# Kernel tuning notes

Measured on AMD Instinct MI355X. Metric: run time of the kernel, lower is better.

The kernel has to match this reference:

```python
import jax, jax.numpy as jnp
import numpy as np

D = 256   # dim = vis_dim = key_channels = value_channels = audio_dim
BT = 64   # batch*time
H = 64
W = 64
L = 32    # audio length

_CONV_NAMES = ["vis_project", "av", "vv", "vo", "ao", "vs_key", "vs_q1", "vs_q2",
               "as_key", "as_q1", "as_q2", "outconv", "aoc"]


def _conv1(x, w, b):
    # pointwise Conv1d: x [B,C,Lx], w [O,C], b [O]
    return jnp.einsum('oc,bcl->bol', w, x) + b[None, :, None]


def _inorm(x, eps=1e-5):
    # InstanceNorm1d (affine=False): normalize over last (spatial) axis
    m = jnp.mean(x, axis=-1, keepdims=True)
    v = jnp.var(x, axis=-1, keepdims=True)
    return (x - m) * jax.lax.rsqrt(v + eps)


def _gelu(x):
    return jax.nn.gelu(x, approximate=False)


def setup_inputs() -> dict:
    key = jax.random.key(0)
    ks = jax.random.split(key, 40)
    inp = {
        "x": jax.random.normal(ks[0], (BT, D, H, W), jnp.float32),
        "audio": jax.random.normal(ks[1], (BT, D, L), jnp.float32),
        "audio_mask": jnp.ones((BT, L, 1), jnp.float32),
    }
    for i, n in enumerate(_CONV_NAMES):
        inp[n + "_w"] = jax.random.normal(ks[3 + 2 * i], (D, D), jnp.float32) * 0.05
        inp[n + "_b"] = jax.random.normal(ks[4 + 2 * i], (D,), jnp.float32) * 0.01
    inp["gate_w1"] = jax.random.normal(ks[30], (D, D), jnp.float32) * 0.05
    inp["gate_w2"] = jax.random.normal(ks[31], (D, D), jnp.float32) * 0.05
    inp["vis_weight"] = jnp.ones((1,), jnp.float32)
    inp["audio_weight"] = jnp.ones((1,), jnp.float32)
    return inp


def reference(x, audio, audio_mask,
              vis_project_w, vis_project_b, av_w, av_b, vv_w, vv_b, vo_w, vo_b,
              ao_w, ao_b, vs_key_w, vs_key_b, vs_q1_w, vs_q1_b, vs_q2_w, vs_q2_b,
              as_key_w, as_key_b, as_q1_w, as_q1_b, as_q2_w, as_q2_b,
              outconv_w, outconv_b, aoc_w, aoc_b, gate_w1, gate_w2,
              vis_weight, audio_weight):
    bt, c, h, w = x.shape
    hw = h * w
    xf = x.reshape(bt, c, hw)                       # [BT,C,HW] (channels-first tokens)
    scale = float(D) ** -0.5                         # key_channels ** -0.5
    maskT = jnp.swapaxes(audio_mask, 1, 2)           # [BT,1,L]

    # vis_project (Conv1d 1x1 + GELU)
    vis = _gelu(_conv1(xf, vis_project_w, vis_project_b))       # [BT,C,HW]

    # ---- AV_Interaction ----
    audio_value = _conv1(audio, av_w, av_b) * maskT              # [BT,C,L]

    # Visual_Sim (kernel=1 -> unfold is identity)
    q1 = _inorm(_conv1(xf, vs_q1_w, vs_q1_b))                    # [BT,C,HW]
    q = _inorm(_conv1(q1, vs_q2_w, vs_q2_b))                     # [BT,C,HW]
    k = _conv1(audio, vs_key_w, vs_key_b) * maskT                # [BT,C,L]
    sim_v = jnp.einsum('bch,bcl->bhl', q, k) * scale             # [BT,HW,L]
    sim_v = sim_v + (10000.0 * maskT - 10000.0)                  # mask keys
    sim_v = jax.nn.softmax(sim_v, axis=-1)
    vw = jax.nn.softmax(vis_weight)[0]                           # softmax over size-1 -> 1.0
    vis_out = jnp.einsum('bhl,bcl->bhc', sim_v * vw, audio_value)  # [BT,HW,C]
    vis_out = _inorm(_conv1(jnp.swapaxes(vis_out, 1, 2), vo_w, vo_b))  # [BT,C,HW]

    # Audio_Sim (kernel=(1,1) -> pad/unfold identity)
    aq = _conv1(_conv1(audio, as_q1_w, as_q1_b), as_q2_w, as_q2_b)  # [BT,C,L]
    ak = _inorm(_conv1(xf, as_key_w, as_key_b))                     # [BT,C,HW]
    aqT = jnp.swapaxes(aq, 1, 2) * audio_mask                       # [BT,L,C]
    sim_a = jnp.einsum('blc,bch->blh', aqT, ak) * scale             # [BT,L,HW]
    sim_a = sim_a + (10000.0 * audio_mask - 10000.0)                # mask query rows
    sim_a = jax.nn.softmax(sim_a, axis=-1)
    aw = jax.nn.softmax(audio_weight)[0]
    vis_value = _inorm(_conv1(xf, vv_w, vv_b))                      # [BT,C,HW]
    audio_o = jnp.einsum('blh,bch->blc', sim_a * aw, vis_value)     # [BT,L,C]
    audio_res = _conv1(jnp.swapaxes(audio_o, 1, 2), ao_w, ao_b)     # [BT,C,L]

    # ---- Dual fusion: vis * vis_weight_map, out_conv ----
    vis = _gelu(_conv1(vis * vis_out, outconv_w, outconv_b))        # [BT,C,HW]
    vis_res = jnp.swapaxes(vis, 1, 2)                               # [BT,HW,C]

    # ---- DAM block: gated residual + audio residual ----
    gate = jnp.tanh(jax.nn.relu(vis_res @ gate_w1.T) @ gate_w2.T)   # [BT,HW,C]
    x_tok = jnp.swapaxes(xf, 1, 2) + gate * vis_res                 # [BT,HW,C]
    x_out = jnp.swapaxes(x_tok, 1, 2).reshape(bt, c, h, w)
    audio_out = audio + _gelu(_conv1(audio_res, aoc_w, aoc_b))      # [BT,C,L]
    return (x_out, audio_out)
```

## Files before the change

kernel.cpp:

```cpp
#include <hip/hip_runtime.h>
#include <math.h>

#define BT 64
#define CH 256
#define HW 4096
#define AL 32
#define SCALE 0.0625f

typedef unsigned short ushort_t;
typedef __bf16 bf16x8 __attribute__((ext_vector_type(8)));
typedef short  short8 __attribute__((ext_vector_type(8)));
typedef float  f32x4  __attribute__((ext_vector_type(4)));

__device__ __forceinline__ float gelu_f(float x){
    return 0.5f*x*(1.0f+erff(x*0.70710678118654752f));
}
__device__ __forceinline__ ushort_t f2bf(float f){
    unsigned int u = __builtin_bit_cast(unsigned int, f);
    u += 0x7fffu + ((u>>16)&1u);
    return (ushort_t)(u>>16);
}
__device__ __forceinline__ float bf2f(ushort_t h){
    unsigned int u = ((unsigned int)h)<<16;
    return __builtin_bit_cast(float, u);
}

#define GLOAD_LDS16(gp, lp) __builtin_amdgcn_global_load_lds( \
    (const __attribute__((address_space(1))) unsigned int*)(gp), \
    (__attribute__((address_space(3))) unsigned int*)(lp), 16, 0, 0)

template<int EPI, int TOUT, int WSTAT>
__global__ __launch_bounds__(256,2)
void gemm_mfma_kernel(const ushort_t* __restrict__ Wb, const float* __restrict__ bias,
                      const ushort_t* __restrict__ Xt, float* __restrict__ Out,
                      ushort_t* __restrict__ OutB,
                      const float* __restrict__ E1, const float* __restrict__ E2,
                      float* __restrict__ St)
{
    __shared__ ushort_t sW[128*32];
    __shared__ ushort_t sX[128*32];
    const int b  = blockIdx.z;
    const int o0 = blockIdx.y*128, p0 = blockIdx.x*128;
    const int tid = threadIdx.x, lane = tid & 63, w = tid >> 6;
    const int wm = w >> 1, wn = w & 1;
    const int rr = lane >> 2;
    const int kk8 = (lane & 3) * 8;

    f32x4 acc[4][4] = {};

    for (int k0 = 0; k0 < CH; k0 += 32) {
        #pragma unroll
        for (int j = 0; j < 2; ++j) {
            const ushort_t* gw = Wb + (size_t)(o0 + w*32 + j*16 + rr)*CH + k0 + kk8;
            GLOAD_LDS16(gw, sW + (size_t)w*1024 + j*512);
        }
        #pragma unroll
        for (int j = 0; j < 2; ++j) {
            const ushort_t* gx = Xt + ((size_t)b*HW + p0 + w*32 + j*16 + rr)*CH + k0 + kk8;
            GLOAD_LDS16(gx, sX + (size_t)w*1024 + j*512);
        }
        __syncthreads();
        bf16x8 af[4], bfr[4];
        #pragma unroll
        for (int mt = 0; mt < 4; ++mt) {
            short8 raw = *(const short8*)(sW + (size_t)(wm*64 + mt*16 + (lane&15))*32 + (lane>>4)*8);
            af[mt] = __builtin_bit_cast(bf16x8, raw);
        }
        #pragma unroll
        for (int nt = 0; nt < 4; ++nt) {
            short8 raw = *(const short8*)(sX + (size_t)(wn*64 + nt*16 + (lane&15))*32 + (lane>>4)*8);
            bfr[nt] = __builtin_bit_cast(bf16x8, raw);
        }
        #pragma unroll
        for (int mt = 0; mt < 4; ++mt)
            #pragma unroll
            for (int nt = 0; nt < 4; ++nt)
                acc[mt][nt] = __builtin_amdgcn_mfma_f32_16x16x32_bf16(af[mt], bfr[nt], acc[mt][nt], 0, 0, 0);
        __syncthreads();
    }

    const int pcol = lane & 15, quad = lane >> 4;
    const size_t obase = (size_t)b*CH*HW;
    if (TOUT == 0) {
        #pragma unroll
        for (int mt = 0; mt < 4; ++mt) {
            #pragma unroll
            for (int r = 0; r < 4; ++r) {
                const int o = o0 + wm*64 + mt*16 + quad*4 + r;
                const float bv = bias ? bias[o] : 0.0f;
                #pragma unroll
                for (int nt = 0; nt < 4; ++nt) {
                    const int p = p0 + wn*64 + nt*16 + pcol;
                    float v = acc[mt][nt][r] + bv;
                    if (EPI == 1) v = gelu_f(v);
                    if (EPI == 2) v = fmaxf(v, 0.0f);
                    if (EPI == 3) {
                        const size_t idx = obase + (size_t)o*HW + p;
                        v = E1[idx] + tanhf(v)*E2[idx];
                    }
                    Out[obase + (size_t)o*HW + p] = v;
                }
            }
        }
    } else if (TOUT == 1) {
        #pragma unroll
        for (int mt = 0; mt < 4; ++mt) {
            const int ob = o0 + wm*64 + mt*16 + quad*4;
            #pragma unroll
            for (int nt = 0; nt < 4; ++nt) {
                const int p = p0 + wn*64 + nt*16 + pcol;
                ushort4 u;
                float v0 = acc[mt][nt][0] + (bias ? bias[ob+0] : 0.f);
                float v1 = acc[mt][nt][1] + (bias ? bias[ob+1] : 0.f);
                float v2 = acc[mt][nt][2] + (bias ? bias[ob+2] : 0.f);
                float v3 = acc[mt][nt][3] + (bias ? bias[ob+3] : 0.f);
                if (EPI == 1) { v0=gelu_f(v0); v1=gelu_f(v1); v2=gelu_f(v2); v3=gelu_f(v3); }
                if (EPI == 2) { v0=fmaxf(v0,0.f); v1=fmaxf(v1,0.f); v2=fmaxf(v2,0.f); v3=fmaxf(v3,0.f); }
                u.x=f2bf(v0); u.y=f2bf(v1); u.z=f2bf(v2); u.w=f2bf(v3);
                *(ushort4*)(OutB + ((size_t)b*HW + p)*CH + ob) = u;
            }
        }
    } else {
        #pragma unroll
        for (int mt = 0; mt < 4; ++mt) {
            const int ob = o0 + wm*64 + mt*16 + quad*4;
            #pragma unroll
            for (int nt = 0; nt < 4; ++nt) {
                const int p = p0 + wn*64 + nt*16 + pcol;
                float v[4];
                #pragma unroll
                for (int r = 0; r < 4; ++r) {
                    float t = acc[mt][nt][r] + (bias ? bias[ob+r] : 0.f);
                    if (EPI == 1) t = gelu_f(t);
                    if (EPI == 2) t = fmaxf(t, 0.f);
                    v[r] = t;
                    Out[obase + (size_t)(ob+r)*HW + p] = t;
                }
                ushort4 u;
                u.x=f2bf(v[0]); u.y=f2bf(v[1]); u.z=f2bf(v[2]); u.w=f2bf(v[3]);
                *(ushort4*)(OutB + ((size_t)b*HW + p)*CH + ob) = u;
            }
        }
    }

    if (WSTAT) {
        float s1[4][4], s2[4][4];
        #pragma unroll
        for (int mt = 0; mt < 4; ++mt) {
            #pragma unroll
            for (int r = 0; r < 4; ++r) {
                const int o = o0 + wm*64 + mt*16 + quad*4 + r;
                const float bv = bias ? bias[o] : 0.0f;
                float a = 0.f, q = 0.f;
                #pragma unroll
                for (int nt = 0; nt < 4; ++nt) {
                    const float v = acc[mt][nt][r] + bv;
                    a += v; q += v*v;
                }
                #pragma unroll
                for (int off = 1; off < 16; off <<= 1) {
                    a += __shfl_xor(a, off);
                    q += __shfl_xor(q, off);
                }
                s1[mt][r] = a; s2[mt][r] = q;
            }
        }
        float* red = (float*)sW;
        __syncthreads();
        if (wn == 0 && pcol == 0) {
            #pragma unroll
            for (int mt = 0; mt < 4; ++mt)
                #pragma unroll
                for (int r = 0; r < 4; ++r) {
                    const int ol = wm*64 + mt*16 + quad*4 + r;
                    red[ol*2] = s1[mt][r]; red[ol*2+1] = s2[mt][r];
                }
        }
        __syncthreads();
        if (wn == 1 && pcol == 0) {
            #pragma unroll
            for (int mt = 0; mt < 4; ++mt)
                #pragma unroll
                for (int r = 0; r < 4; ++r) {
                    const int ol = wm*64 + mt*16 + quad*4 + r;
                    const int o = o0 + ol;
                    atomicAdd(&St[((size_t)b*CH + o)*2],   red[ol*2]   + s1[mt][r]);
                    atomicAdd(&St[((size_t)b*CH + o)*2+1], red[ol*2+1] + s2[mt][r]);
                }
        }
    }
}

__global__ __launch_bounds__(256)
void zero_kernel(float* __restrict__ p)
{
    p[blockIdx.x*256 + threadIdx.x] = 0.f;
}

__global__ __launch_bounds__(256)
void stats_finalize_kernel(float* __restrict__ St)
{
    const int row = blockIdx.x*256 + threadIdx.x;
    const float s1 = St[(size_t)row*2], s2 = St[(size_t)row*2+1];
    const float mean = s1 * (1.0f/HW);
    const float var  = s2 * (1.0f/HW) - mean*mean;
    St[(size_t)row*2]   = mean;
    St[(size_t)row*2+1] = rsqrtf(var + 1e-5f);
}

template<int MODE>
__global__ __launch_bounds__(256)
void transpose_bf16_kernel(const float* __restrict__ Xa, const ushort_t* __restrict__ Mul,
                           const float* __restrict__ St, ushort_t* __restrict__ Out)
{
    __shared__ float sT[32][33];
    const int b = blockIdx.z, c0 = blockIdx.y*32, p0 = blockIdx.x*32;
    const int tid = threadIdx.x;
    {
        const int cr = tid >> 3, pq = (tid & 7)*4;
        float4 v = *(const float4*)(Xa + ((size_t)b*CH + c0 + cr)*HW + p0 + pq);
        if (MODE >= 1) {
            const float m = St[((size_t)b*CH + c0 + cr)*2];
            const float r = St[((size_t)b*CH + c0 + cr)*2+1];
            v.x = (v.x-m)*r; v.y = (v.y-m)*r; v.z = (v.z-m)*r; v.w = (v.w-m)*r;
        }
        sT[cr][pq+0]=v.x; sT[cr][pq+1]=v.y; sT[cr][pq+2]=v.z; sT[cr][pq+3]=v.w;
    }
    __syncthreads();
    {
        const int pr = tid >> 3, cq = (tid & 7)*4;
        const size_t oidx = ((size_t)b*HW + p0 + pr)*CH + c0 + cq;
        float v0 = sT[cq+0][pr], v1 = sT[cq+1][pr], v2 = sT[cq+2][pr], v3 = sT[cq+3][pr];
        if (MODE == 2) {
            const ushort4 m = *(const ushort4*)(Mul + oidx);
            v0 *= bf2f(m.x); v1 *= bf2f(m.y); v2 *= bf2f(m.z); v3 *= bf2f(m.w);
        }
        ushort4 u; u.x=f2bf(v0); u.y=f2bf(v1); u.z=f2bf(v2); u.w=f2bf(v3);
        *(ushort4*)(Out + oidx) = u;
    }
}

__global__ __launch_bounds__(256)
void wconv_kernel(const float* w0, const float* w1, const float* w2, const float* w3,
                  const float* w4, const float* w5, const float* w6, const float* w7,
                  const float* w8, ushort_t* __restrict__ Wb)
{
    const float* src;
    switch (blockIdx.y) {
        case 0: src=w0; break; case 1: src=w1; break; case 2: src=w2; break;
        case 3: src=w3; break; case 4: src=w4; break; case 5: src=w5; break;
        case 6: src=w6; break; case 7: src=w7; break; default: src=w8; break;
    }
    const int i = (blockIdx.x*256 + threadIdx.x)*4;
    const float4 v = *(const float4*)(src + i);
    ushort4 u; u.x=f2bf(v.x); u.y=f2bf(v.y); u.z=f2bf(v.z); u.w=f2bf(v.w);
    *(ushort4*)(Wb + (size_t)blockIdx.y*65536 + i) = u;
}

template<int EPI, int TR>
__global__ __launch_bounds__(256)
void conv_l_kernel(const float* __restrict__ W, const float* __restrict__ bias,
                   const float* __restrict__ X, float* __restrict__ Out,
                   const float* __restrict__ Mask, const float* __restrict__ Resid,
                   const float* __restrict__ St)
{
    const int b = blockIdx.x;
    const int o = blockIdx.y*8 + (threadIdx.x>>5);
    const int l = threadIdx.x & 31;
    const float* xb = X + (size_t)b*CH*AL + l;
    const float* wr = W + (size_t)o*CH;
    float acc = bias ? bias[o] : 0.0f;
    #pragma unroll 8
    for (int c=0;c<CH;++c) acc = fmaf(wr[c], xb[(size_t)c*AL], acc);
    if (EPI==1) acc *= Mask[b*AL + l];
    if (EPI==4) acc *= Mask[b*AL + l] * St[((size_t)b*CH + o)*2+1] * SCALE;
    if (EPI==2) {
        const size_t oi = (size_t)b*CH*AL + (size_t)o*AL + l;
        acc = Resid[oi] + gelu_f(acc);
    }
    if (TR == 0) Out[(size_t)b*CH*AL + (size_t)o*AL + l] = acc;
    else         Out[((size_t)b*AL + l)*CH + o] = acc;
}

__global__ __launch_bounds__(256)
void lbias_kernel(const float* __restrict__ Kn, const float* __restrict__ St,
                  float* __restrict__ Lb)
{
    const int b = blockIdx.x, tid = threadIdx.x;
    const int l = tid & 31, g = tid >> 5;
    float s = 0.f;
    #pragma unroll 8
    for (int cc=0; cc<32; ++cc){
        const int c = g*32 + cc;
        s += St[((size_t)b*CH + c)*2] * Kn[((size_t)b*CH + c)*AL + l];
    }
    __shared__ float red[8][32];
    red[g][l] = s;
    __syncthreads();
    if (tid < 32){
        float t = 0.f;
        #pragma unroll
        for (int gg=0; gg<8; ++gg) t += red[gg][tid];
        Lb[b*AL + tid] = -t;
    }
}

__device__ __forceinline__ void attn_loadq(f32x4 (&dst)[8], const float* Qb, int kc){
    #pragma unroll
    for (int kk=0;kk<8;++kk)
        dst[kk] = *(const f32x4*)(Qb + (size_t)(kc*8+kk)*HW);
}
__device__ __forceinline__ void attn_fma(float (&s)[4][4], const f32x4 (&q)[8],
                                         const float* sKV, int kc, int lq){
    #pragma unroll
    for (int kk=0;kk<8;++kk){
        const f32x4 kv = *(const f32x4*)&sKV[(kc*8+kk)*32 + lq*4];
        #pragma unroll
        for (int i=0;i<4;++i)
            #pragma unroll
            for (int j=0;j<4;++j)
                s[i][j] = fmaf(q[kk][i], kv[j], s[i][j]);
    }
}

__global__ __launch_bounds__(256,3)
void attn_v_kernel(const float* __restrict__ Q, const float* __restrict__ Kn,
                   const float* __restrict__ AVt, const float* __restrict__ Lb,
                   const float* __restrict__ Mask, ushort_t* __restrict__ OutB)
{
    __shared__ float sKV[8192];
    __shared__ float sP[32*128];
    __shared__ float sBias[32];
    const int b  = blockIdx.y;
    const int p0 = blockIdx.x * 128;
    const int tid = threadIdx.x;
    const int pg = tid >> 3;
    const int lq = tid & 7;

    #pragma unroll
    for (int ii=0; ii<8; ++ii){
        const int fi = ii*256 + tid;
        *(f32x4*)&sKV[fi*4] = *(const f32x4*)(Kn + (size_t)b*CH*AL + (size_t)fi*4);
    }
    if (tid < 32) sBias[tid] = Lb[b*AL + tid] + 10000.f*Mask[b*AL + tid] - 10000.f;
    __syncthreads();

    const float* Qb = Q + (size_t)b*CH*HW + p0 + pg*4;
    float s[4][4] = {};
    {
        f32x4 qa[8], qb2[8];
        attn_loadq(qa, Qb, 0);
        for (int kc = 0; kc < 32; kc += 2){
            attn_loadq(qb2, Qb, kc+1);
            attn_fma(s, qa, sKV, kc, lq);
            if (kc+2 < 32) attn_loadq(qa, Qb, kc+2);
            attn_fma(s, qb2, sKV, kc+1, lq);
        }
    }
    __syncthreads();

    #pragma unroll
    for (int j=0;j<4;++j)
        *(f32x4*)&sP[(lq*4+j)*128 + pg*4] = (f32x4){s[0][j], s[1][j], s[2][j], s[3][j]};
    #pragma unroll
    for (int ii=0; ii<8; ++ii){
        const int fi = ii*256 + tid;
        *(f32x4*)&sKV[fi*4] = *(const f32x4*)(AVt + (size_t)b*AL*CH + (size_t)fi*4);
    }
    __syncthreads();

    {
        const int p = tid >> 1, lh = tid & 1;
        float v[16];
        #pragma unroll
        for (int jj=0;jj<16;++jj) v[jj] = sP[(lh*16+jj)*128 + p] + sBias[lh*16+jj];
        float m = v[0];
        #pragma unroll
        for (int jj=1;jj<16;++jj) m = fmaxf(m, v[jj]);
        m = fmaxf(m, __shfl_xor(m, 1));
        float z = 0.f;
        #pragma unroll
        for (int jj=0;jj<16;++jj){ v[jj] = expf(v[jj]-m); z += v[jj]; }
        z += __shfl_xor(z, 1);
        const float rz = 1.f/z;
        #pragma unroll
        for (int jj=0;jj<16;++jj) sP[(lh*16+jj)*128 + p] = v[jj]*rz;
    }
    __syncthreads();

    const int cg = lq;
    ushort_t* Ob = OutB + ((size_t)b*HW + p0 + pg*4)*CH;
    #pragma unroll 1
    for (int c0=0; c0<CH; c0+=64){
        float acc[4][8] = {};
        #pragma unroll
        for (int k=0;k<32;++k){
            const f32x4 pv = *(const f32x4*)&sP[k*128 + pg*4];
            const f32x4 a0 = *(const f32x4*)&sKV[k*256 + c0 + cg*8];
            const f32x4 a1 = *(const f32x4*)&sKV[k*256 + c0 + cg*8 + 4];
            #pragma unroll
            for (int i=0;i<4;++i){
                acc[i][0]=fmaf(pv[i],a0[0],acc[i][0]); acc[i][1]=fmaf(pv[i],a0[1],acc[i][1]);
                acc[i][2]=fmaf(pv[i],a0[2],acc[i][2]); acc[i][3]=fmaf(pv[i],a0[3],acc[i][3]);
                acc[i][4]=fmaf(pv[i],a1[0],acc[i][4]); acc[i][5]=fmaf(pv[i],a1[1],acc[i][5]);
                acc[i][6]=fmaf(pv[i],a1[2],acc[i][6]); acc[i][7]=fmaf(pv[i],a1[3],acc[i][7]);
            }
        }
        #pragma unroll
        for (int i=0;i<4;++i){
            short8 u;
            #pragma unroll
            for (int j=0;j<8;++j) u[j] = (short)f2bf(acc[i][j]);
            *(short8*)(Ob + (size_t)i*CH + c0 + cg*8) = u;
        }
    }
}

__global__ __launch_bounds__(256)
void sima_raw_kernel(const float* __restrict__ AQ, const float* __restrict__ AK,
                     const float* __restrict__ Mask, const float* __restrict__ St,
                     float* __restrict__ Sraw)
{
    __shared__ float sAQ[CH*AL];
    const int b = blockIdx.y;
    const int p = blockIdx.x*256 + threadIdx.x;
    const int tid = threadIdx.x;
    #pragma unroll
    for (int i=0;i<32;++i){
        const int idx = tid + 256*i;
        sAQ[idx] = AQ[(size_t)b*CH*AL + idx] * Mask[b*AL + (idx&31)] * SCALE
                 * St[((size_t)b*CH + (idx>>5))*2+1];
    }
    __syncthreads();
    float s[32];
    #pragma unroll
    for (int l=0;l<32;++l) s[l]=0.f;
    const float* akb = AK + (size_t)b*CH*HW + p;
    for (int c=0;c<CH;++c){
        const float a = akb[(size_t)c*HW];
        const float* qr = &sAQ[c*32];
        #pragma unroll
        for (int l=0;l<32;++l) s[l] = fmaf(qr[l], a, s[l]);
    }
    float* outp = Sraw + (size_t)b*AL*HW + p;
    #pragma unroll
    for (int l=0;l<32;++l) outp[(size_t)l*HW] = s[l];
}

__global__ __launch_bounds__(256)
void sima_stats_kernel(const float* __restrict__ Sraw, float2* __restrict__ Stats)
{
    const size_t base = (size_t)blockIdx.x * HW;
    const int tid = threadIdx.x;
    float v[16];
    #pragma unroll
    for (int i=0;i<4;++i){
        const float4 t = *(const float4*)(Sraw + base + tid*4 + i*1024);
        v[i*4+0]=t.x; v[i*4+1]=t.y; v[i*4+2]=t.z; v[i*4+3]=t.w;
    }
    float m = v[0];
    #pragma unroll
    for (int i=1;i<16;++i) m = fmaxf(m, v[i]);
    #pragma unroll
    for (int off=1; off<64; off<<=1) m = fmaxf(m, __shfl_xor(m, off));
    __shared__ float rm[4], rz[4];
    if ((tid&63)==0) rm[tid>>6]=m;
    __syncthreads();
    m = fmaxf(fmaxf(rm[0],rm[1]), fmaxf(rm[2],rm[3]));
    float z=0.f;
    #pragma unroll
    for (int i=0;i<16;++i) z += expf(v[i]-m);
    #pragma unroll
    for (int off=1; off<64; off<<=1) z += __shfl_xor(z, off);
    if ((tid&63)==0) rz[tid>>6]=z;
    __syncthreads();
    if (tid==0) Stats[blockIdx.x] = make_float2(m, 1.0f/(rz[0]+rz[1]+rz[2]+rz[3]));
}

__global__ __launch_bounds__(256)
void sima_pv_kernel(const float* __restrict__ Sraw, const float2* __restrict__ SmStats,
                    const float* __restrict__ VV, const float* __restrict__ ChSt,
                    float* __restrict__ AO)
{
    __shared__ float sA[32*33];
    __shared__ float sB[64*36];
    __shared__ float sM[32], sR[32];
    const int b  = blockIdx.x >> 2;
    const int c0 = (blockIdx.x & 3) * 64;
    const int tid = threadIdx.x;
    if (tid < 32){
        const float2 st = SmStats[b*AL + tid];
        sM[tid] = st.x; sR[tid] = st.y;
    }
    __syncthreads();
    const int lh = tid & 15;
    const int cq = tid >> 4;
    const int lr = tid >> 3, k4 = (tid & 7) * 4;
    float acc[2][4] = {{0.f,0.f,0.f,0.f},{0.f,0.f,0.f,0.f}};
    for (int p0=0; p0<HW; p0+=32){
        {
            const float4 t = *(const float4*)(Sraw + ((size_t)b*AL + lr)*HW + p0 + k4);
            const float mm = sM[lr], rr2 = sR[lr];
            sA[lr*33 + k4+0] = expf(t.x-mm)*rr2;
            sA[lr*33 + k4+1] = expf(t.y-mm)*rr2;
            sA[lr*33 + k4+2] = expf(t.z-mm)*rr2;
            sA[lr*33 + k4+3] = expf(t.w-mm)*rr2;
        }
        #pragma unroll
        for (int i=0;i<2;++i){
            const int cc = (tid>>3) + 32*i;
            *(float4*)&sB[cc*36 + k4] = *(const float4*)(VV + ((size_t)b*CH + c0 + cc)*HW + p0 + k4);
        }
        __syncthreads();
        #pragma unroll
        for (int kk=0;kk<32;++kk){
            const float a0 = sA[lh*33 + kk];
            const float a1 = sA[(lh+16)*33 + kk];
            #pragma unroll
            for (int j=0;j<4;++j){
                const float bb = sB[(cq*4+j)*36 + kk];
                acc[0][j] = fmaf(a0, bb, acc[0][j]);
                acc[1][j] = fmaf(a1, bb, acc[1][j]);
            }
        }
        __syncthreads();
    }
    #pragma unroll
    for (int j=0;j<4;++j){
        const int c = c0 + cq*4 + j;
        const float m0 = ChSt[((size_t)b*CH + c)*2];
        const float r0 = ChSt[((size_t)b*CH + c)*2+1];
        AO[((size_t)b*CH + c)*AL + lh]      = (acc[0][j]-m0)*r0;
        AO[((size_t)b*CH + c)*AL + lh + 16] = (acc[1][j]-m0)*r0;
    }
}

extern "C" void kernel_launch(void* const* d_in, const int* in_sizes, int n_in,
                              void* d_out, int out_size, void* d_ws, size_t ws_size,
                              hipStream_t stream)
{
    (void)in_sizes; (void)n_in; (void)out_size; (void)ws_size;
    const float* x     = (const float*)d_in[0];
    const float* audio = (const float*)d_in[1];
    const float* amask = (const float*)d_in[2];
    const float* vis_project_w = (const float*)d_in[3];
    const float* vis_project_b = (const float*)d_in[4];
    const float* av_w = (const float*)d_in[5];
    const float* av_b = (const float*)d_in[6];
    const float* vv_w = (const float*)d_in[7];
    const float* vv_b = (const float*)d_in[8];
    const float* vo_w = (const float*)d_in[9];
    const float* vo_b = (const float*)d_in[10];
    const float* ao_w = (const float*)d_in[11];
    const float* ao_b = (const float*)d_in[12];
    const float* vs_key_w = (const float*)d_in[13];
    const float* vs_key_b = (const float*)d_in[14];
    const float* vs_q1_w = (const float*)d_in[15];
    const float* vs_q1_b = (const float*)d_in[16];
    const float* vs_q2_w = (const float*)d_in[17];
    const float* vs_q2_b = (const float*)d_in[18];
    const float* as_key_w = (const float*)d_in[19];
    const float* as_key_b = (const float*)d_in[20];
    const float* as_q1_w = (const float*)d_in[21];
    const float* as_q1_b = (const float*)d_in[22];
    const float* as_q2_w = (const float*)d_in[23];
    const float* as_q2_b = (const float*)d_in[24];
    const float* outconv_w = (const float*)d_in[25];
    const float* outconv_b = (const float*)d_in[26];
    const float* aoc_w = (const float*)d_in[27];
    const float* aoc_b = (const float*)d_in[28];
    const float* gate_w1 = (const float*)d_in[29];
    const float* gate_w2 = (const float*)d_in[30];

    float* out_x = (float*)d_out;
    float* out_a = out_x + (size_t)BT*CH*HW;
    float* B     = out_x;

    const size_t BIG = (size_t)BT*CH*HW;
    ushort_t* Xt   = (ushort_t*)d_ws;
    ushort_t* VISB = Xt + BIG;
    float*  A     = (float*)(VISB + BIG);
    float*  SIMA  = A + BIG;
    float2* STATS = (float2*)(SIMA + (size_t)BT*AL*HW);
    float*  S0 = (float*)(STATS + BT*AL);
    float*  S1 = S0 + (size_t)BT*CH*AL;
    float*  S2 = S1 + (size_t)BT*CH*AL;
    float*  S3 = S2 + (size_t)BT*CH*AL;
    float*  S4 = S3 + (size_t)BT*CH*AL;
    ushort_t* Wb = (ushort_t*)(S4 + (size_t)BT*CH*AL);
    float*  SA = (float*)(Wb + (size_t)9*65536);
    float*  SB = SA + (size_t)2*BT*CH;
    float*  LB = SB + (size_t)2*BT*CH;

    dim3 b256(256);
    dim3 gW(64, 9);
    dim3 gL(BT, CH/8);
    dim3 gT(HW/32, CH/32, BT);
    dim3 gG(HW/128, CH/128, BT);
    dim3 gAttnV(HW/128, BT);
    dim3 gSimA(HW/256, BT);
    dim3 gZ(2*BT*CH/256);
    dim3 gF(BT*CH/256);

    #define WSLOT(i) (Wb + (size_t)(i)*65536)
    hipLaunchKernelGGL(wconv_kernel, gW, b256, 0, stream,
                       vs_q1_w, as_key_w, vv_w, vis_project_w, vs_q2_w, vo_w, outconv_w, gate_w1, gate_w2, Wb);
    hipLaunchKernelGGL((conv_l_kernel<1,1>), gL, b256, 0, stream, av_w, av_b, audio, S0, amask, nullptr, nullptr);
    hipLaunchKernelGGL((conv_l_kernel<0,0>), gL, b256, 0, stream, as_q1_w, as_q1_b, audio, S3, nullptr, nullptr, nullptr);
    hipLaunchKernelGGL((conv_l_kernel<0,0>), gL, b256, 0, stream, as_q2_w, as_q2_b, S3, S2, nullptr, nullptr, nullptr);
    hipLaunchKernelGGL((transpose_bf16_kernel<0>), gT, b256, 0, stream, x, nullptr, nullptr, Xt);
    hipLaunchKernelGGL(zero_kernel, gZ, b256, 0, stream, SA);
    hipLaunchKernelGGL((gemm_mfma_kernel<0,0,1>), gG, b256, 0, stream, WSLOT(0), vs_q1_b, Xt, A, nullptr, nullptr, nullptr, SA);
    hipLaunchKernelGGL(stats_finalize_kernel, gF, b256, 0, stream, SA);
    hipLaunchKernelGGL(zero_kernel, gZ, b256, 0, stream, SB);
    hipLaunchKernelGGL((gemm_mfma_kernel<0,0,1>), gG, b256, 0, stream, WSLOT(1), as_key_b, Xt, B, nullptr, nullptr, nullptr, SB);
    hipLaunchKernelGGL(stats_finalize_kernel, gF, b256, 0, stream, SB);
    hipLaunchKernelGGL(sima_raw_kernel, gSimA, b256, 0, stream, S2, B, amask, SB, SIMA);
    hipLaunchKernelGGL(sima_stats_kernel, dim3(BT*AL), b256, 0, stream, SIMA, STATS);
    hipLaunchKernelGGL(zero_kernel, gZ, b256, 0, stream, SB);
    hipLaunchKernelGGL((gemm_mfma_kernel<0,0,1>), gG, b256, 0, stream, WSLOT(2), vv_b, Xt, B, nullptr, nullptr, nullptr, SB);
    hipLaunchKernelGGL(stats_finalize_kernel, gF, b256, 0, stream, SB);
    hipLaunchKernelGGL(sima_pv_kernel, dim3(BT*4), b256, 0, stream, SIMA, STATS, B, SB, S4);
    hipLaunchKernelGGL((conv_l_kernel<0,0>), gL, b256, 0, stream, ao_w, ao_b, S4, S3, nullptr, nullptr, nullptr);
    hipLaunchKernelGGL((conv_l_kernel<2,0>), gL, b256, 0, stream, aoc_w, aoc_b, S3, out_a, nullptr, audio, nullptr);
    hipLaunchKernelGGL((gemm_mfma_kernel<1,1,0>), gG, b256, 0, stream, WSLOT(3), vis_project_b, Xt, nullptr, VISB, nullptr, nullptr, nullptr);
    hipLaunchKernelGGL((transpose_bf16_kernel<1>), gT, b256, 0, stream, A, nullptr, SA, Xt);
    hipLaunchKernelGGL(zero_kernel, gZ, b256, 0, stream, SA);
    hipLaunchKernelGGL((gemm_mfma_kernel<0,0,1>), gG, b256, 0, stream, WSLOT(4), vs_q2_b, Xt, B, nullptr, nullptr, nullptr, SA);
    hipLaunchKernelGGL(stats_finalize_kernel, gF, b256, 0, stream, SA);
    hipLaunchKernelGGL((conv_l_kernel<4,0>), gL, b256, 0, stream, vs_key_w, vs_key_b, audio, S1, amask, nullptr, SA);
    hipLaunchKernelGGL(lbias_kernel, dim3(BT), b256, 0, stream, S1, SA, LB);
    hipLaunchKernelGGL(attn_v_kernel, gAttnV, b256, 0, stream, B, S1, S0, LB, amask, Xt);
    hipLaunchKernelGGL(zero_kernel, gZ, b256, 0, stream, SA);
    hipLaunchKernelGGL((gemm_mfma_kernel<0,0,1>), gG, b256, 0, stream, WSLOT(5), vo_b, Xt, B, nullptr, nullptr, nullptr, SA);
    hipLaunchKernelGGL(stats_finalize_kernel, gF, b256, 0, stream, SA);
    hipLaunchKernelGGL((transpose_bf16_kernel<2>), gT, b256, 0, stream, B, VISB, SA, Xt);
    hipLaunchKernelGGL((gemm_mfma_kernel<1,2,0>), gG, b256, 0, stream, WSLOT(6), outconv_b, Xt, A, VISB, nullptr, nullptr, nullptr);
    hipLaunchKernelGGL((gemm_mfma_kernel<2,1,0>), gG, b256, 0, stream, WSLOT(7), nullptr, VISB, nullptr, Xt, nullptr, nullptr, nullptr);
    hipLaunchKernelGGL((gemm_mfma_kernel<3,0,0>), gG, b256, 0, stream, WSLOT(8), nullptr, Xt, out_x, nullptr, x, A, nullptr);
    #undef WSLOT
}
```

Measured before the change: 2.954 ms.

## Restructure attention-V kernel: register softmax, bf16 probabilities, staged coalesced output

Reworks attn_v_kernel to process 256 tokens per block, each thread computing 4 tokens × 8 audio keys so the softmax stays in registers with shuffle reductions, removing an LDS round-trip and a barrier. Kn and AVt are loaded once up front into separate shared buffers. Probabilities are stored in LDS as bf16. Output tiles are staged through XOR-swizzled shared memory so global writes are fully coalesced rows. This costs more LDS and registers (occupancy hint drops from 3 to 2 blocks) and rounds probabilities to bf16 before the PV product.

```diff
diff --git a/kernel.cpp b/kernel.cpp
--- a/kernel.cpp
+++ b/kernel.cpp
@@ -305,114 +305,148 @@
     }
 }
 
-__device__ __forceinline__ void attn_loadq(f32x4 (&dst)[8], const float* Qb, int kc){
-    #pragma unroll
-    for (int kk=0;kk<8;++kk)
-        dst[kk] = *(const f32x4*)(Qb + (size_t)(kc*8+kk)*HW);
-}
-__device__ __forceinline__ void attn_fma(float (&s)[4][4], const f32x4 (&q)[8],
-                                         const float* sKV, int kc, int lq){
-    #pragma unroll
-    for (int kk=0;kk<8;++kk){
-        const f32x4 kv = *(const f32x4*)&sKV[(kc*8+kk)*32 + lq*4];
-        #pragma unroll
-        for (int i=0;i<4;++i)
-            #pragma unroll
-            for (int j=0;j<4;++j)
-                s[i][j] = fmaf(q[kk][i], kv[j], s[i][j]);
-    }
-}
-
-__global__ __launch_bounds__(256,3)
+__global__ __launch_bounds__(256,2)
 void attn_v_kernel(const float* __restrict__ Q, const float* __restrict__ Kn,
                    const float* __restrict__ AVt, const float* __restrict__ Lb,
                    const float* __restrict__ Mask, ushort_t* __restrict__ OutB)
 {
-    __shared__ float sKV[8192];
-    __shared__ float sP[32*128];
-    __shared__ float sBias[32];
+    __shared__ float smemf[20480];
+    float*    sKn  = smemf;
+    ushort_t* sOut = (ushort_t*)smemf;
+    ushort_t* sPb  = (ushort_t*)(smemf + 8192);
+    float*    sAV  = smemf + 12288;
+
     const int b  = blockIdx.y;
-    const int p0 = blockIdx.x * 128;
-    const int tid = threadIdx.x;
-    const int pg = tid >> 3;
-    const int lq = tid & 7;
+    const int p0 = blockIdx.x * 256;
+    const int tid = threadIdx.x, lane = tid & 63, w = tid >> 6;
+    const int pg = lane >> 2;
+    const int lq = lane & 3;
 
     #pragma unroll
     for (int ii=0; ii<8; ++ii){
         const int fi = ii*256 + tid;
-        *(f32x4*)&sKV[fi*4] = *(const f32x4*)(Kn + (size_t)b*CH*AL + (size_t)fi*4);
-    }
-    if (tid < 32) sBias[tid] = Lb[b*AL + tid] + 10000.f*Mask[b*AL + tid] - 10000.f;
-    __syncthreads();
-
-    const float* Qb = Q + (size_t)b*CH*HW + p0 + pg*4;
-    float s[4][4] = {};
+        *(f32x4*)&sKn[fi*4] = *(const f32x4*)(Kn + (size_t)b*CH*AL + (size_t)fi*4);
+        *(f32x4*)&sAV[fi*4] = *(const f32x4*)(AVt + (size_t)b*AL*CH + (size_t)fi*4);
+    }
+    float bias[8];
+    #pragma unroll
+    for (int j=0;j<8;++j){
+        const int l = lq*8 + j;
+        bias[j] = Lb[b*AL + l] + 10000.f*Mask[b*AL + l] - 10000.f;
+    }
+    __syncthreads();
+
+    const float* Qb = Q + (size_t)b*CH*HW + p0 + w*64 + pg*4;
+    float s[4][8] = {};
     {
         f32x4 qa[8], qb2[8];
-        attn_loadq(qa, Qb, 0);
+        #pragma unroll
+        for (int kk=0;kk<8;++kk) qa[kk] = *(const f32x4*)(Qb + (size_t)kk*HW);
         for (int kc = 0; kc < 32; kc += 2){
-            attn_loadq(qb2, Qb, kc+1);
-            attn_fma(s, qa, sKV, kc, lq);
-            if (kc+2 < 32) attn_loadq(qa, Qb, kc+2);
-            attn_fma(s, qb2, sKV, kc+1, lq);
-        }
-    }
-    __syncthreads();
-
-    #pragma unroll
-    for (int j=0;j<4;++j)
-        *(f32x4*)&sP[(lq*4+j)*128 + pg*4] = (f32x4){s[0][j], s[1][j], s[2][j], s[3][j]};
-    #pragma unroll
-    for (int ii=0; ii<8; ++ii){
-        const int fi = ii*256 + tid;
-        *(f32x4*)&sKV[fi*4] = *(const f32x4*)(AVt + (size_t)b*AL*CH + (size_t)fi*4);
-    }
-    __syncthreads();
+            #pragma unroll
+            for (int kk=0;kk<8;++kk) qb2[kk] = *(const f32x4*)(Qb + (size_t)((kc+1)*8+kk)*HW);
+            #pragma unroll
+            for (int kk=0;kk<8;++kk){
+                const int c = kc*8 + kk;
+                const f32x4 kn0 = *(const f32x4*)&sKn[c*32 + lq*8];
+                const f32x4 kn1 = *(const f32x4*)&sKn[c*32 + lq*8 + 4];
+                #pragma unroll
+                for (int i=0;i<4;++i){
+                    s[i][0]=fmaf(qa[kk][i],kn0[0],s[i][0]); s[i][1]=fmaf(qa[kk][i],kn0[1],s[i][1]);
+                    s[i][2]=fmaf(qa[kk][i],kn0[2],s[i][2]); s[i][3]=fmaf(qa[kk][i],kn0[3],s[i][3]);
+                    s[i][4]=fmaf(qa[kk][i],kn1[0],s[i][4]); s[i][5]=fmaf(qa[kk][i],kn1[1],s[i][5]);
+                    s[i][6]=fmaf(qa[kk][i],kn1[2],s[i][6]); s[i][7]=fmaf(qa[kk][i],kn1[3],s[i][7]);
+                }
+            }
+            if (kc+2 < 32){
+                #pragma unroll
+                for (int kk=0;kk<8;++kk) qa[kk] = *(const f32x4*)(Qb + (size_t)((kc+2)*8+kk)*HW);
+            }
+            #pragma unroll
+            for (int kk=0;kk<8;++kk){
+                const int c = (kc+1)*8 + kk;
+                const f32x4 kn0 = *(const f32x4*)&sKn[c*32 + lq*8];
+                const f32x4 kn1 = *(const f32x4*)&sKn[c*32 + lq*8 + 4];
+                #pragma unroll
+                for (int i=0;i<4;++i){
+                    s[i][0]=fmaf(qb2[kk][i],kn0[0],s[i][0]); s[i][1]=fmaf(qb2[kk][i],kn0[1],s[i][1]);
+                    s[i][2]=fmaf(qb2[kk][i],kn0[2],s[i][2]); s[i][3]=fmaf(qb2[kk][i],kn0[3],s[i][3]);
+                    s[i][4]=fmaf(qb2[kk][i],kn1[0],s[i][4]); s[i][5]=fmaf(qb2[kk][i],kn1[1],s[i][5]);
+                    s[i][6]=fmaf(qb2[kk][i],kn1[2],s[i][6]); s[i][7]=fmaf(qb2[kk][i],kn1[3],s[i][7]);
+                }
+            }
+        }
+    }
+
+    #pragma unroll
+    for (int i=0;i<4;++i){
+        #pragma unroll
+        for (int j=0;j<8;++j) s[i][j] += bias[j];
+        float m = s[i][0];
+        #pragma unroll
+        for (int j=1;j<8;++j) m = fmaxf(m, s[i][j]);
+        m = fmaxf(m, __shfl_xor(m, 1));
+        m = fmaxf(m, __shfl_xor(m, 2));
+        float z = 0.f;
+        #pragma unroll
+        for (int j=0;j<8;++j){ s[i][j] = expf(s[i][j]-m); z += s[i][j]; }
+        z += __shfl_xor(z, 1);
+        z += __shfl_xor(z, 2);
+        const float rz = 1.f/z;
+        #pragma unroll
+        for (int j=0;j<8;++j) s[i][j] *= rz;
+    }
 
     {
-        const int p = tid >> 1, lh = tid & 1;
-        float v[16];
-        #pragma unroll
-        for (int jj=0;jj<16;++jj) v[jj] = sP[(lh*16+jj)*128 + p] + sBias[lh*16+jj];
-        float m = v[0];
-        #pragma unroll
-        for (int jj=1;jj<16;++jj) m = fmaxf(m, v[jj]);
-        m = fmaxf(m, __shfl_xor(m, 1));
-        float z = 0.f;
-        #pragma unroll
-        for (int jj=0;jj<16;++jj){ v[jj] = expf(v[jj]-m); z += v[jj]; }
-        z += __shfl_xor(z, 1);
-        const float rz = 1.f/z;
-        #pragma unroll
-        for (int jj=0;jj<16;++jj) sP[(lh*16+jj)*128 + p] = v[jj]*rz;
-    }
-    __syncthreads();
-
-    const int cg = lq;
-    ushort_t* Ob = OutB + ((size_t)b*HW + p0 + pg*4)*CH;
-    #pragma unroll 1
-    for (int c0=0; c0<CH; c0+=64){
-        float acc[4][8] = {};
-        #pragma unroll
+        const int tok = w*64 + pg*4;
+        #pragma unroll
+        for (int j=0;j<8;++j){
+            const int l = lq*8 + j;
+            unsigned u01 = (unsigned)f2bf(s[0][j]) | ((unsigned)f2bf(s[1][j])<<16);
+            unsigned u23 = (unsigned)f2bf(s[2][j]) | ((unsigned)f2bf(s[3][j])<<16);
+            *(unsigned*)&sPb[l*256 + tok]     = u01;
+            *(unsigned*)&sPb[l*256 + tok + 2] = u23;
+        }
+    }
+    __syncthreads();
+
+    const int tokL = tid >> 2;
+    const int cq   = tid & 3;
+    for (int t0 = 0; t0 < 4; ++t0){
+        const int tok = t0*64 + tokL;
+        float acc[8][8] = {};
         for (int k=0;k<32;++k){
-            const f32x4 pv = *(const f32x4*)&sP[k*128 + pg*4];
-            const f32x4 a0 = *(const f32x4*)&sKV[k*256 + c0 + cg*8];
-            const f32x4 a1 = *(const f32x4*)&sKV[k*256 + c0 + cg*8 + 4];
-            #pragma unroll
-            for (int i=0;i<4;++i){
-                acc[i][0]=fmaf(pv[i],a0[0],acc[i][0]); acc[i][1]=fmaf(pv[i],a0[1],acc[i][1]);
-                acc[i][2]=fmaf(pv[i],a0[2],acc[i][2]); acc[i][3]=fmaf(pv[i],a0[3],acc[i][3]);
-                acc[i][4]=fmaf(pv[i],a1[0],acc[i][4]); acc[i][5]=fmaf(pv[i],a1[1],acc[i][5]);
-                acc[i][6]=fmaf(pv[i],a1[2],acc[i][6]); acc[i][7]=fmaf(pv[i],a1[3],acc[i][7]);
-            }
-        }
-        #pragma unroll
-        for (int i=0;i<4;++i){
+            const float pv = bf2f(sPb[k*256 + tok]);
+            #pragma unroll
+            for (int ch=0;ch<8;++ch){
+                const f32x4 a0 = *(const f32x4*)&sAV[k*256 + ch*32 + cq*8];
+                const f32x4 a1 = *(const f32x4*)&sAV[k*256 + ch*32 + cq*8 + 4];
+                acc[ch][0]=fmaf(pv,a0[0],acc[ch][0]); acc[ch][1]=fmaf(pv,a0[1],acc[ch][1]);
+                acc[ch][2]=fmaf(pv,a0[2],acc[ch][2]); acc[ch][3]=fmaf(pv,a0[3],acc[ch][3]);
+                acc[ch][4]=fmaf(pv,a1[0],acc[ch][4]); acc[ch][5]=fmaf(pv,a1[1],acc[ch][5]);
+                acc[ch][6]=fmaf(pv,a1[2],acc[ch][6]); acc[ch][7]=fmaf(pv,a1[3],acc[ch][7]);
+            }
+        }
+        #pragma unroll
+        for (int ch=0;ch<8;++ch){
             short8 u;
             #pragma unroll
-            for (int j=0;j<8;++j) u[j] = (short)f2bf(acc[i][j]);
-            *(short8*)(Ob + (size_t)i*CH + c0 + cg*8) = u;
-        }
+            for (int j=0;j<8;++j) u[j] = (short)f2bf(acc[ch][j]);
+            const int chunk = (ch*4 + cq) ^ (tokL & 7);
+            *(short8*)&sOut[tokL*256 + chunk*8] = u;
+        }
+        __syncthreads();
+        {
+            ushort_t* Ob = OutB + ((size_t)b*HW + p0 + t0*64)*CH;
+            const int chunk = tid & 31;
+            #pragma unroll
+            for (int ss=0;ss<8;++ss){
+                const int row = ss*8 + (tid>>5);
+                short8 v = *(const short8*)&sOut[row*256 + ((chunk ^ (row&7))*8)];
+                *(short8*)(Ob + (size_t)row*CH + chunk*8) = v;
+            }
+        }
+        __syncthreads();
     }
 }
 
@@ -597,7 +631,7 @@
     dim3 gL(BT, CH/8);
     dim3 gT(HW/32, CH/32, BT);
     dim3 gG(HW/128, CH/128, BT);
-    dim3 gAttnV(HW/128, BT);
+    dim3 gAttnV(HW/256, BT);
     dim3 gSimA(HW/256, BT);
     dim3 gZ(2*BT*CH/256);
     dim3 gF(BT*CH/256);
```

New measurement: 2.716 ms. 1.09x faster.
